# Optimization experiments

Measured on AMD Instinct MI355X. Metric: run time of the kernel, lower is better.

The kernel has to match this reference:

```python
import jax, jax.numpy as jnp
import numpy as np

N = 100_000          # NEURON_COUNT (scaled)
INPUT_SIZE = 1024    # input neurons occupy indices [0, INPUT_SIZE)
OUTPUT_SIZE = 256    # output neurons occupy indices [N-OUTPUT_SIZE, N)
E = 10_000_000       # SYNAPSE_RATIO * N
STEPS = 3


def setup_inputs() -> dict:
    key = jax.random.key(0)
    k1, k2, k3, k4, k5 = jax.random.split(key, 5)
    x = jax.random.normal(k1, (INPUT_SIZE,), dtype=jnp.float32)
    synapse_weights = jax.random.normal(k2, (E,), dtype=jnp.float32)
    neuron_biases = jax.random.normal(k3, (N - INPUT_SIZE,), dtype=jnp.float32)
    synapse_src = jax.random.randint(k4, (E,), 0, N, dtype=jnp.int64) if jax.config.jax_enable_x64 else jax.random.randint(k4, (E,), 0, N, dtype=jnp.int32)
    synapse_dst = jax.random.randint(k5, (E,), 0, N, dtype=jnp.int64) if jax.config.jax_enable_x64 else jax.random.randint(k5, (E,), 0, N, dtype=jnp.int32)
    return {
        "x": x,
        "synapse_weights": synapse_weights,
        "neuron_biases": neuron_biases,
        "synapse_src": synapse_src,
        "synapse_dst": synapse_dst,
    }


def reference(x, synapse_weights, neuron_biases, synapse_src, synapse_dst):
    # Initial state: zeros everywhere, inputs injected at the first INPUT_SIZE slots.
    v = jnp.zeros((N,), dtype=x.dtype).at[:INPUT_SIZE].set(x.reshape(-1))
    # tanh applied to all neurons except outputs (last OUTPUT_SIZE indices)
    tanh_mask = jnp.arange(N) < (N - OUTPUT_SIZE)
    for _ in range(STEPS):
        # vectorized gather-multiply-scatter: next[to] += v[from] * w  (one segment_sum)
        msg = v[synapse_src] * synapse_weights                       # [E]
        nxt = jax.ops.segment_sum(msg, synapse_dst, num_segments=N)  # [N]
        # biases added to all non-input neurons
        nxt = nxt.at[INPUT_SIZE:].add(neuron_biases)
        # tanh everywhere except output neurons
        v = jnp.where(tanh_mask, jnp.tanh(nxt), nxt)
    return v[N - OUTPUT_SIZE:]
```

## Files before the change

kernel.cpp:

```cpp
#include <hip/hip_runtime.h>

#define N_NEURONS   100000
#define INPUT_SIZE  1024
#define OUTPUT_SIZE 256
#define E_SYN       10000000
#define STEPS       3

#define RANGES      8
#define BIN         12500
#define SCAT_BLK    512
#define CBLK        64
#define CAP         1280000
#define B_CNT       800
#define CH          12500
#define VEC4        (E_SYN / 4)

__global__ void init_all(const float* __restrict__ x, float* __restrict__ v,
                         int* __restrict__ gcur) {
    int i = blockIdx.x * blockDim.x + threadIdx.x;
    if (i < N_NEURONS) v[i] = (i < INPUT_SIZE) ? x[i] : 0.0f;
    if (i < RANGES) gcur[i] = 0;
}

__global__ void reorder_partition(const float* __restrict__ w,
                                  const int*   __restrict__ src,
                                  const int*   __restrict__ dst,
                                  float* __restrict__ w_s,
                                  int2*  __restrict__ sd_s,
                                  int*   __restrict__ gcur) {
    __shared__ int cnt[RANGES][9];
    __shared__ int cursor[RANGES];
    const int tid = threadIdx.x;
    const int l8 = tid & 7;
    if (tid < RANGES * 9) ((int*)cnt)[tid] = 0;
    __syncthreads();

    const int beg = blockIdx.x * CH;
    const int end = beg + CH;
    for (int e = beg + tid; e < end; e += blockDim.x) {
        int r = dst[e] / BIN;
        atomicAdd(&cnt[r][l8], 1);
    }
    __syncthreads();
    if (tid < RANGES) {
        int s = 0;
#pragma unroll
        for (int l = 0; l < 8; ++l) s += cnt[tid][l];
        cursor[tid] = tid * CAP + atomicAdd(&gcur[tid], s);
    }
    __syncthreads();
    for (int e = beg + tid; e < end; e += blockDim.x) {
        int d = dst[e];
        int r = d / BIN;
        int pos = atomicAdd(&cursor[r], 1);
        w_s[pos]  = w[e];
        sd_s[pos] = make_int2(src[e], d);
    }
}

__global__ void scatter_sorted(const float* __restrict__ w_s,
                               const int2*  __restrict__ sd_s,
                               const int*   __restrict__ gcur,
                               const float* __restrict__ v,
                               float*       __restrict__ partials) {
    __shared__ float bins[BIN];
    const int r  = blockIdx.x / CBLK;
    const int c  = blockIdx.x % CBLK;
    const int lo = r * BIN;
    for (int j = threadIdx.x; j < BIN; j += blockDim.x) bins[j] = 0.0f;
    __syncthreads();

    const int beg = r * CAP;
    const int end = beg + gcur[r];
    const int stride = CBLK * blockDim.x;
    for (int u = beg + c * blockDim.x + threadIdx.x; u < end; u += stride) {
        int2  sd = sd_s[u];
        float m  = v[sd.x] * w_s[u];
        atomicAdd(&bins[sd.y - lo], m);
    }
    __syncthreads();

    float* o = partials + (size_t)(r * CBLK + c) * BIN;
    for (int j = threadIdx.x; j < BIN; j += blockDim.x) o[j] = bins[j];
}

__global__ void reduce_update(const float* __restrict__ partials,
                              const float* __restrict__ bias,
                              float* __restrict__ v,
                              float* __restrict__ out,
                              int C, int write_out) {
    int i4 = 4 * (blockIdx.x * blockDim.x + threadIdx.x);
    if (i4 >= N_NEURONS) return;
    const int r = i4 / BIN;
    const int j = i4 - r * BIN;
    const float* base = partials + ((size_t)r * C) * BIN + j;
    float4 acc = {0.f, 0.f, 0.f, 0.f};
    for (int c = 0; c < C; ++c) {
        float4 p = *(const float4*)(base + (size_t)c * BIN);
        acc.x += p.x; acc.y += p.y; acc.z += p.z; acc.w += p.w;
    }
    float av[4] = {acc.x, acc.y, acc.z, acc.w};
#pragma unroll
    for (int k = 0; k < 4; ++k) {
        int i = i4 + k;
        float val = av[k] + ((i >= INPUT_SIZE) ? bias[i - INPUT_SIZE] : 0.0f);
        float nv  = (i < N_NEURONS - OUTPUT_SIZE) ? tanhf(val) : val;
        v[i] = nv;
        if (write_out && i >= N_NEURONS - OUTPUT_SIZE)
            out[i - (N_NEURONS - OUTPUT_SIZE)] = val;
    }
}

__global__ void init_state_fb(const float* __restrict__ x, float* __restrict__ v) {
    int i = blockIdx.x * blockDim.x + threadIdx.x;
    if (i < N_NEURONS) v[i] = (i < INPUT_SIZE) ? x[i] : 0.0f;
}
__global__ void scatter_binned(const float* __restrict__ w,
                               const int*   __restrict__ src,
                               const int*   __restrict__ dst,
                               const float* __restrict__ v,
                               float*       __restrict__ partials,
                               int C) {
    __shared__ float bins[BIN];
    const int r = blockIdx.x / C;
    const int c = blockIdx.x % C;
    const int lo = r * BIN;
    const int hi = lo + BIN;
    for (int j = threadIdx.x; j < BIN; j += blockDim.x) bins[j] = 0.0f;
    __syncthreads();
    const int4*   src4 = (const int4*)src;
    const int4*   dst4 = (const int4*)dst;
    const float4* w4v  = (const float4*)w;
    const int stride = C * blockDim.x;
    for (int u = c * blockDim.x + threadIdx.x; u < VEC4; u += stride) {
        const int4   s4 = src4[u];
        const int4   d4 = dst4[u];
        const float4 wv = w4v[u];
        int   s[4] = {s4.x, s4.y, s4.z, s4.w};
        int   d[4] = {d4.x, d4.y, d4.z, d4.w};
        float ww[4] = {wv.x, wv.y, wv.z, wv.w};
#pragma unroll
        for (int k = 0; k < 4; ++k)
            if (d[k] >= lo && d[k] < hi)
                atomicAdd(&bins[d[k] - lo], v[s[k]] * ww[k]);
    }
    __syncthreads();
    float* o = partials + ((size_t)(r * C + c)) * BIN;
    for (int j = threadIdx.x; j < BIN; j += blockDim.x) o[j] = bins[j];
}

extern "C" void kernel_launch(void* const* d_in, const int* in_sizes, int n_in,
                              void* d_out, int out_size, void* d_ws, size_t ws_size,
                              hipStream_t stream) {
    const float* x    = (const float*)d_in[0];
    const float* w    = (const float*)d_in[1];
    const float* bias = (const float*)d_in[2];
    const int*   src  = (const int*)d_in[3];
    const int*   dst  = (const int*)d_in[4];
    float* out = (float*)d_out;

    const int blk = 256;
    const int grid_n   = (N_NEURONS + blk - 1) / blk;
    const int red_grid = (N_NEURONS / 4 + blk - 1) / blk;

    float* v        = (float*)d_ws;
    float* partials = v + N_NEURONS;
    float* w_s      = partials + (size_t)RANGES * CBLK * BIN;
    int2*  sd_s     = (int2*)(w_s + (size_t)RANGES * CAP);
    int*   gcur     = (int*)(sd_s + (size_t)RANGES * CAP);
    size_t need = (size_t)(gcur + RANGES) - (size_t)d_ws;

    if (ws_size >= need) {
        init_all<<<grid_n, blk, 0, stream>>>(x, v, gcur);
        reorder_partition<<<B_CNT, blk, 0, stream>>>(w, src, dst, w_s, sd_s, gcur);
        for (int s = 0; s < STEPS; ++s) {
            scatter_sorted<<<RANGES * CBLK, SCAT_BLK, 0, stream>>>(
                w_s, sd_s, gcur, v, partials);
            reduce_update<<<red_grid, blk, 0, stream>>>(
                partials, bias, v, out, CBLK, s == STEPS - 1 ? 1 : 0);
        }
    } else {
        long C = (long)(ws_size / 4 / N_NEURONS) - 1;
        if (C > 64) C = 64;
        if (C < 1) C = 1;
        float* part_fb = v + N_NEURONS;
        init_state_fb<<<grid_n, blk, 0, stream>>>(x, v);
        for (int s = 0; s < STEPS; ++s) {
            scatter_binned<<<RANGES * (int)C, SCAT_BLK, 0, stream>>>(
                w, src, dst, v, part_fb, (int)C);
            reduce_update<<<red_grid, blk, 0, stream>>>(
                part_fb, bias, v, out, (int)C, s == STEPS - 1 ? 1 : 0);
        }
    }
}
```

Measured before the change: 472.2 us.

## Pack synapse records into 8 bytes and use wave-aggregated partitioning

```diff
diff --git a/kernel.cpp b/kernel.cpp
--- a/kernel.cpp
+++ b/kernel.cpp
@@ -9,10 +9,11 @@
 #define RANGES      8
 #define BIN         12500
 #define SCAT_BLK    512
-#define CBLK        64
+#define CBLK        96
 #define CAP         1280000
-#define B_CNT       800
-#define CH          12500
+#define RB_BLK      256
+#define CH          5000
+#define B_CNT       2000
 #define VEC4        (E_SYN / 4)
 
 __global__ void init_all(const float* __restrict__ x, float* __restrict__ v,
@@ -25,63 +26,85 @@
 __global__ void reorder_partition(const float* __restrict__ w,
                                   const int*   __restrict__ src,
                                   const int*   __restrict__ dst,
-                                  float* __restrict__ w_s,
-                                  int2*  __restrict__ sd_s,
-                                  int*   __restrict__ gcur) {
-    __shared__ int cnt[RANGES][9];
+                                  int2* __restrict__ recs,
+                                  int*  __restrict__ gcur) {
+    __shared__ int cnt[RANGES];
     __shared__ int cursor[RANGES];
-    const int tid = threadIdx.x;
-    const int l8 = tid & 7;
-    if (tid < RANGES * 9) ((int*)cnt)[tid] = 0;
-    __syncthreads();
-
-    const int beg = blockIdx.x * CH;
-    const int end = beg + CH;
-    for (int e = beg + tid; e < end; e += blockDim.x) {
-        int r = dst[e] / BIN;
-        atomicAdd(&cnt[r][l8], 1);
-    }
-    __syncthreads();
-    if (tid < RANGES) {
-        int s = 0;
-#pragma unroll
-        for (int l = 0; l < 8; ++l) s += cnt[tid][l];
-        cursor[tid] = tid * CAP + atomicAdd(&gcur[tid], s);
-    }
-    __syncthreads();
-    for (int e = beg + tid; e < end; e += blockDim.x) {
-        int d = dst[e];
-        int r = d / BIN;
-        int pos = atomicAdd(&cursor[r], 1);
-        w_s[pos]  = w[e];
-        sd_s[pos] = make_int2(src[e], d);
-    }
-}
-
-__global__ void scatter_sorted(const float* __restrict__ w_s,
-                               const int2*  __restrict__ sd_s,
-                               const int*   __restrict__ gcur,
-                               const float* __restrict__ v,
-                               float*       __restrict__ partials) {
+    const int tid  = threadIdx.x;
+    const int lane = tid & 63;
+    const unsigned long long ltmask = (1ull << lane) - 1ull;
+    if (tid < RANGES) cnt[tid] = 0;
+    __syncthreads();
+
+    const int beg  = blockIdx.x * CH;
+    const int endx = beg + CH;
+    const int ITER = (CH + RB_BLK - 1) / RB_BLK;
+
+    int wcnt = 0;
+    for (int it = 0; it < ITER; ++it) {
+        int  e  = beg + it * RB_BLK + tid;
+        bool ok = (e < endx);
+        int  r  = ok ? (dst[e] / BIN) : -1;
+#pragma unroll
+        for (int rr = 0; rr < RANGES; ++rr) {
+            unsigned long long mask = __ballot(r == rr);
+            if (lane == rr) wcnt += __popcll(mask);
+        }
+    }
+    if (lane < RANGES) atomicAdd(&cnt[lane], wcnt);
+    __syncthreads();
+    if (tid < RANGES) cursor[tid] = tid * CAP + atomicAdd(&gcur[tid], cnt[tid]);
+    __syncthreads();
+
+    for (int it = 0; it < ITER; ++it) {
+        int  e  = beg + it * RB_BLK + tid;
+        bool ok = (e < endx);
+        int  d  = ok ? dst[e] : 0;
+        int  r  = ok ? (d / BIN) : -1;
+        int  pos = 0;
+#pragma unroll
+        for (int rr = 0; rr < RANGES; ++rr) {
+            unsigned long long mask = __ballot(r == rr);
+            int tot = __popcll(mask);
+            int b = 0;
+            if (lane == rr) b = atomicAdd(&cursor[rr], tot);
+            b = __shfl(b, rr, 64);
+            if (r == rr) pos = b + __popcll(mask & ltmask);
+        }
+        if (ok) {
+            int code = (src[e] << 14) | (d - r * BIN);
+            recs[pos] = make_int2(code, __float_as_int(w[e]));
+        }
+    }
+}
+
+__global__ __launch_bounds__(SCAT_BLK) void scatter_sorted(
+        const int2* __restrict__ recs,
+        const int*  __restrict__ gcur,
+        const float* __restrict__ v,
+        float* __restrict__ partials) {
     __shared__ float bins[BIN];
-    const int r  = blockIdx.x / CBLK;
-    const int c  = blockIdx.x % CBLK;
-    const int lo = r * BIN;
-    for (int j = threadIdx.x; j < BIN; j += blockDim.x) bins[j] = 0.0f;
-    __syncthreads();
-
-    const int beg = r * CAP;
-    const int end = beg + gcur[r];
-    const int stride = CBLK * blockDim.x;
-    for (int u = beg + c * blockDim.x + threadIdx.x; u < end; u += stride) {
-        int2  sd = sd_s[u];
-        float m  = v[sd.x] * w_s[u];
-        atomicAdd(&bins[sd.y - lo], m);
-    }
-    __syncthreads();
-
+    const int r = blockIdx.x / CBLK;
+    const int c = blockIdx.x % CBLK;
+    for (int j = threadIdx.x; j < BIN; j += SCAT_BLK) bins[j] = 0.0f;
+    __syncthreads();
+
+    const int cnt   = gcur[r];
+    const int npair = cnt >> 1;
+    const int4* base4 = (const int4*)(recs + (size_t)r * CAP);
+    const int stride = CBLK * SCAT_BLK;
+    for (int u = c * SCAT_BLK + threadIdx.x; u < npair; u += stride) {
+        int4 p = base4[u];
+        atomicAdd(&bins[p.x & 16383], v[p.x >> 14] * __int_as_float(p.y));
+        atomicAdd(&bins[p.z & 16383], v[p.z >> 14] * __int_as_float(p.w));
+    }
+    if ((cnt & 1) && c == 0 && threadIdx.x == 0) {
+        int2 p = recs[(size_t)r * CAP + cnt - 1];
+        atomicAdd(&bins[p.x & 16383], v[p.x >> 14] * __int_as_float(p.y));
+    }
+    __syncthreads();
     float* o = partials + (size_t)(r * CBLK + c) * BIN;
-    for (int j = threadIdx.x; j < BIN; j += blockDim.x) o[j] = bins[j];
+    for (int j = threadIdx.x; j < BIN; j += SCAT_BLK) o[j] = bins[j];
 }
 
 __global__ void reduce_update(const float* __restrict__ partials,
@@ -165,17 +188,16 @@
 
     float* v        = (float*)d_ws;
     float* partials = v + N_NEURONS;
-    float* w_s      = partials + (size_t)RANGES * CBLK * BIN;
-    int2*  sd_s     = (int2*)(w_s + (size_t)RANGES * CAP);
-    int*   gcur     = (int*)(sd_s + (size_t)RANGES * CAP);
-    size_t need = (size_t)(gcur + RANGES) - (size_t)d_ws;
+    int2*  recs     = (int2*)(partials + (size_t)RANGES * CBLK * BIN);
+    int*   gcur     = (int*)(recs + (size_t)RANGES * CAP);
+    size_t need = (size_t)((char*)(gcur + RANGES) - (char*)d_ws);
 
     if (ws_size >= need) {
         init_all<<<grid_n, blk, 0, stream>>>(x, v, gcur);
-        reorder_partition<<<B_CNT, blk, 0, stream>>>(w, src, dst, w_s, sd_s, gcur);
+        reorder_partition<<<B_CNT, RB_BLK, 0, stream>>>(w, src, dst, recs, gcur);
         for (int s = 0; s < STEPS; ++s) {
             scatter_sorted<<<RANGES * CBLK, SCAT_BLK, 0, stream>>>(
-                w_s, sd_s, gcur, v, partials);
+                recs, gcur, v, partials);
             reduce_update<<<red_grid, blk, 0, stream>>>(
                 partials, bias, v, out, CBLK, s == STEPS - 1 ? 1 : 0);
         }
```

After: 461.1 us. 2.3% less time.
